# Performance work log

Hardware: AMD Instinct MI355X
Metric: run time of the kernel (lower is better)

The kernel has to match this reference:

```python
import jax, jax.numpy as jnp
import numpy as np

DIMS = [512, 256, 256, 256, 256, 256, 128, 128, 64, 40]
N_NODES = 100000
N_EDGES = 3200000


def setup_inputs() -> dict:
    key = jax.random.key(0)
    ks = jax.random.split(key, 4 + 2 * 9)
    inp = {
        "x": jax.random.normal(ks[0], (N_NODES, DIMS[0]), dtype=jnp.float32),
        "edge_src": jax.random.randint(ks[1], (N_EDGES,), 0, N_NODES, dtype=jnp.int32),
        "edge_dst": jax.random.randint(ks[2], (N_EDGES,), 0, N_NODES, dtype=jnp.int32),
        "edge_weight": jax.random.uniform(ks[3], (N_EDGES,), dtype=jnp.float32) / 32.0,
    }
    for i in range(9):
        fi, fo = DIMS[i], DIMS[i + 1]
        scale = 1.0 / np.sqrt(fi)
        inp[f"W{i+1}"] = jax.random.normal(ks[4 + 2 * i], (fi, fo), dtype=jnp.float32) * scale
        inp[f"b{i+1}"] = jax.random.normal(ks[5 + 2 * i], (fo,), dtype=jnp.float32) * scale
    return inp


def _gcn_layer(h, W, b, src, dst, w, n_nodes):
    # support = h @ W; out[i] = sum over edges (i <- j) of w * support[j] + b
    support = h @ W                          # [N, fo]
    msgs = w[:, None] * support[src]         # [E, fo] gather
    agg = jax.ops.segment_sum(msgs, dst, num_segments=n_nodes)  # [N, fo] scatter-add
    return agg + b


def reference(x, edge_src, edge_dst, edge_weight,
              W1, b1, W2, b2, W3, b3, W4, b4, W5, b5,
              W6, b6, W7, b7, W8, b8, W9, b9):
    n = x.shape[0]
    Ws = (W1, W2, W3, W4, W5, W6, W7, W8, W9)
    bs = (b1, b2, b3, b4, b5, b6, b7, b8, b9)
    h = x
    for i in range(8):  # layers 1..8 with ReLU
        h = jax.nn.relu(_gcn_layer(h, Ws[i], bs[i], edge_src, edge_dst, edge_weight, n))
    h = _gcn_layer(h, Ws[8], bs[8], edge_src, edge_dst, edge_weight, n)
    return jax.nn.log_softmax(h, axis=1)
```

## Files before the change

### kernel.cpp

```cpp
#include <hip/hip_runtime.h>
#include <cstdint>
#include <cstddef>

typedef __attribute__((ext_vector_type(8))) short bf16x8;
typedef __attribute__((ext_vector_type(4))) float f32x4;

static inline int cdiv(int a, int b) { return (a + b - 1) / b; }

__device__ inline unsigned short f2bf(float f) {
    union { float f; unsigned int u; } v; v.f = f;
    unsigned int u = v.u;
    return (unsigned short)((u + 0x7FFFu + ((u >> 16) & 1u)) >> 16);
}
__device__ inline float bf2f(unsigned short b) {
    union { unsigned int u; float f; } v; v.u = ((unsigned int)b) << 16;
    return v.f;
}

__device__ inline void fma16u(float* a, const int4& d, float ws) {
    const unsigned int dw[4] = {(unsigned)d.x, (unsigned)d.y, (unsigned)d.z, (unsigned)d.w};
#pragma unroll
    for (int w = 0; w < 4; ++w) {
        a[w * 4 + 0] += ws * (float)(dw[w] & 0xFFu);
        a[w * 4 + 1] += ws * (float)((dw[w] >> 8) & 0xFFu);
        a[w * 4 + 2] += ws * (float)((dw[w] >> 16) & 0xFFu);
        a[w * 4 + 3] += ws * (float)(dw[w] >> 24);
    }
}


struct TW {
    const float* W[9];
    int K[9];
    int N[9];
    int base[10];
    int nN;
};

__global__ __launch_bounds__(256) void prep_kernel(TW tw, unsigned short* __restrict__ Wt,
                                                   int* __restrict__ deg,
                                                   int* __restrict__ bucketCursor, int total) {
    int t = blockIdx.x * 256 + threadIdx.x;
    if (t < tw.nN) deg[t] = 0;
    if (t < 8) bucketCursor[t] = 0;
    if (t >= total) return;
    int l = 0;
#pragma unroll
    for (int i = 1; i <= 8; ++i)
        if (t >= tw.base[i]) l = i;
    int loc = t - tw.base[l];
    int K = tw.K[l], N = tw.N[l];
    int n = loc / K, k = loc - n * K;
    float v = (n < N) ? tw.W[l][(size_t)k * N + n] : 0.f;
    Wt[t] = f2bf(v);
}


#define PB_BLOCKS 2048

__global__ __launch_bounds__(256) void partition_v2(
        const int* __restrict__ src, const int* __restrict__ dst,
        const float* __restrict__ w,
        int* __restrict__ bucketCursor, int4* __restrict__ staging,
        int bucketCap, int nE, int nN) {
    __shared__ int cnt[8];
    __shared__ int cur[8];
    const int tid = threadIdx.x;
    const int lane = tid & 63;
    const int perBlock = (nE + (int)gridDim.x - 1) / (int)gridDim.x;
    const int begE = blockIdx.x * perBlock;
    const int endE = (begE + perBlock < nE) ? begE + perBlock : nE;
    if (begE >= endE) return;
    if (tid < 8) cnt[tid] = 0;
    __syncthreads();
    for (int i = begE + tid; i < endE; i += 256) {
        int d = dst[i];
        int b = (int)(((long long)d * 8) / nN);
#pragma unroll
        for (int bb = 0; bb < 8; ++bb) {
            unsigned long long mask = __ballot(b == bb);
            if (mask && lane == (__ffsll(mask) - 1))
                atomicAdd(&cnt[bb], (int)__popcll(mask));
        }
    }
    __syncthreads();
    if (tid < 8) cur[tid] = atomicAdd(&bucketCursor[tid], cnt[tid]);
    __syncthreads();
    for (int i = begE + tid; i < endE; i += 256) {
        int d = dst[i], s = src[i];
        float wv = w[i];
        int b = (int)(((long long)d * 8) / nN);
        int pos = 0;
#pragma unroll
        for (int bb = 0; bb < 8; ++bb) {
            unsigned long long mask = __ballot(b == bb);
            int leader = mask ? (__ffsll(mask) - 1) : 0;
            int base_bb = 0;
            if (mask && lane == leader) base_bb = atomicAdd(&cur[bb], (int)__popcll(mask));
            base_bb = __shfl(base_bb, leader);
            if (b == bb) pos = base_bb + (int)__popcll(mask & ((1ull << lane) - 1ull));
        }
        staging[(size_t)b * bucketCap + pos] = make_int4(d, s, __float_as_int(wv), 0);
    }
}


#define DC_BPB 32

__global__ __launch_bounds__(256) void deg_count(const int4* __restrict__ staging,
                                                 const int* __restrict__ bucketCnt,
                                                 int bucketCap, int* __restrict__ deg, int nN) {
    __shared__ int hist[12512];
    int bucket = blockIdx.x & 7;
    int chunk = blockIdx.x >> 3;
    int cnt = bucketCnt[bucket];
    int lo = (int)(((long long)bucket * nN + 7) / 8);
    int hi = (int)(((long long)(bucket + 1) * nN + 7) / 8);
    if (hi > nN) hi = nN;
    int span = hi - lo;
    for (int i = threadIdx.x; i < span; i += 256) hist[i] = 0;
    __syncthreads();
    const int4* st = staging + (size_t)bucket * bucketCap;
    for (int i = chunk * 256 + threadIdx.x; i < cnt; i += DC_BPB * 256)
        atomicAdd(&hist[st[i].x - lo], 1);
    __syncthreads();
    for (int i = threadIdx.x; i < span; i += 256) {
        int v = hist[i];
        if (v) atomicAdd(&deg[lo + i], v);
    }
}


__global__ __launch_bounds__(256) void scan_part(const int* __restrict__ deg,
                                                 int* __restrict__ partials, int n) {
    __shared__ int sdata[256];
    int tid = threadIdx.x;
    int base = blockIdx.x * 1024;
    int local = 0;
#pragma unroll
    for (int i = 0; i < 4; ++i) {
        int idx = base + tid * 4 + i;
        local += (idx < n) ? deg[idx] : 0;
    }
    sdata[tid] = local;
    __syncthreads();
    for (int off = 128; off; off >>= 1) {
        if (tid < off) sdata[tid] += sdata[tid + off];
        __syncthreads();
    }
    if (tid == 0) partials[blockIdx.x] = sdata[0];
}

__global__ __launch_bounds__(256) void scan_final2(const int* __restrict__ deg,
                                                   const int* __restrict__ partials,
                                                   int* __restrict__ rowptr,
                                                   int* __restrict__ cursor, int n, int nb) {
    __shared__ int ps[128];
    __shared__ int sdata[256];
    int tid = threadIdx.x;
    if (tid < 128) ps[tid] = (tid < nb) ? partials[tid] : 0;
    __syncthreads();
    for (int off = 1; off < 128; off <<= 1) {
        int t = (tid < 128 && tid >= off) ? ps[tid - off] : 0;
        __syncthreads();
        if (tid < 128) ps[tid] += t;
        __syncthreads();
    }
    int base = (blockIdx.x == 0) ? 0 : ps[blockIdx.x - 1];
    if (blockIdx.x == 0 && tid == 0) rowptr[n] = ps[nb - 1];
    int bb = blockIdx.x * 1024;
    int vals[4];
    int local = 0;
#pragma unroll
    for (int i = 0; i < 4; ++i) {
        int idx = bb + tid * 4 + i;
        vals[i] = (idx < n) ? deg[idx] : 0;
        local += vals[i];
    }
    sdata[tid] = local;
    __syncthreads();
    for (int off = 1; off < 256; off <<= 1) {
        int t = (tid >= off) ? sdata[tid - off] : 0;
        __syncthreads();
        sdata[tid] += t;
        __syncthreads();
    }
    int run = sdata[tid] - local + base;
#pragma unroll
    for (int i = 0; i < 4; ++i) {
        int idx = bb + tid * 4 + i;
        if (idx < n) { rowptr[idx] = run; cursor[idx] = run; }
        run += vals[i];
    }
}


__global__ __launch_bounds__(256) void scatter_b(const int4* __restrict__ staging,
                                                 const int* __restrict__ bucketCnt,
                                                 int bucketCap, int* __restrict__ cursor,
                                                 int2* __restrict__ ep, int blocksPerBucket) {
    int bucket = blockIdx.x & 7;
    int chunk = blockIdx.x >> 3;
    int cnt = bucketCnt[bucket];
    const int4* st = staging + (size_t)bucket * bucketCap;
    for (int i = chunk * 256 + threadIdx.x; i < cnt; i += blocksPerBucket * 256) {
        int4 r = st[i];
        int pos = atomicAdd(&cursor[r.x], 1);
        ep[pos] = make_int2(r.y, r.z);
    }
}


template <int BN, bool AF32, int OUTQ>
__global__ __launch_bounds__(256) void gemm_mfma(const void* __restrict__ Av,
                                                 const unsigned short* __restrict__ Bt,
                                                 void* __restrict__ Cv,
                                                 float* __restrict__ scArr,
                                                 int M, int K, int N) {
    constexpr int BM = 128, BK = 64;
    __shared__ unsigned short As[BM * BK];
    __shared__ unsigned short Bs[BN * BK];
    const int tid = threadIdx.x;
    const int lane = tid & 63, wid = tid >> 6;
    const int m0 = blockIdx.x * BM, n0 = blockIdx.y * BN;

    constexpr int WN = (BN == 128) ? 2 : 1;
    constexpr int WTM = (BN == 128) ? 64 : 32;
    constexpr int FM = WTM / 16, FN = 4;
    const int wm = (wid / WN) * WTM;
    const int wn = (wid % WN) * 64;
    const int g = lane >> 4, r16 = lane & 15;

    const unsigned short* A16 = (const unsigned short*)Av;
    const float* A32 = (const float*)Av;

    f32x4 acc[FM][FN] = {};

    for (int k0 = 0; k0 < K; k0 += BK) {
        if constexpr (AF32) {
#pragma unroll
            for (int it = 0; it < 4; ++it) {
                int c = it * 256 + tid;
                int r = c >> 3, kc = c & 7;
                int gm = m0 + r;
                bf16x8 val;
                if (gm < M) {
                    const float* p = A32 + (size_t)gm * K + k0 + kc * 8;
                    float4 v0 = *reinterpret_cast<const float4*>(p);
                    float4 v1 = *reinterpret_cast<const float4*>(p + 4);
                    val[0] = (short)f2bf(v0.x); val[1] = (short)f2bf(v0.y);
                    val[2] = (short)f2bf(v0.z); val[3] = (short)f2bf(v0.w);
                    val[4] = (short)f2bf(v1.x); val[5] = (short)f2bf(v1.y);
                    val[6] = (short)f2bf(v1.z); val[7] = (short)f2bf(v1.w);
                } else {
#pragma unroll
                    for (int j = 0; j < 8; ++j) val[j] = 0;
                }
                *reinterpret_cast<bf16x8*>(&As[r * BK + kc * 8]) = val;
            }
        } else {
#pragma unroll
            for (int c = 0; c < 4; ++c) {
                int base = wid * 32 + c * 8;
                int row = base + (lane >> 3), kc = lane & 7;
                const unsigned short* gp = A16 + (size_t)(m0 + row) * K + k0 + kc * 8;
                __builtin_amdgcn_global_load_lds(
                    (const __attribute__((address_space(1))) void*)gp,
                    (__attribute__((address_space(3))) void*)&As[base * BK], 16, 0, 0);
            }
        }
        {
            constexpr int BCALLS = (BN * BK) / (512 * 4);
#pragma unroll
            for (int c = 0; c < BCALLS; ++c) {
                int base = wid * (BN / 4) + c * 8;
                int row = base + (lane >> 3), kc = lane & 7;
                const unsigned short* gp = Bt + (size_t)(n0 + row) * K + k0 + kc * 8;
                __builtin_amdgcn_global_load_lds(
                    (const __attribute__((address_space(1))) void*)gp,
                    (__attribute__((address_space(3))) void*)&Bs[base * BK], 16, 0, 0);
            }
        }
        __syncthreads();
#pragma unroll
        for (int ks = 0; ks < 2; ++ks) {
            bf16x8 af[FM], bfr[FN];
#pragma unroll
            for (int i = 0; i < FM; ++i)
                af[i] = *reinterpret_cast<const bf16x8*>(&As[(wm + i * 16 + r16) * BK + ks * 32 + g * 8]);
#pragma unroll
            for (int j = 0; j < FN; ++j)
                bfr[j] = *reinterpret_cast<const bf16x8*>(&Bs[(wn + j * 16 + r16) * BK + ks * 32 + g * 8]);
#pragma unroll
            for (int i = 0; i < FM; ++i)
#pragma unroll
                for (int j = 0; j < FN; ++j)
                    acc[i][j] = __builtin_amdgcn_mfma_f32_16x16x32_bf16(af[i], bfr[j], acc[i][j], 0, 0, 0);
        }
        __syncthreads();
    }

    if constexpr (OUTQ == 1) {
        __shared__ float rmax2[2][BM];
        const int wc = wid % WN;
        unsigned char* C8 = (unsigned char*)Cv;
#pragma unroll
        for (int i = 0; i < FM; ++i) {
#pragma unroll
            for (int r = 0; r < 4; ++r) {
                float m = 0.f;
#pragma unroll
                for (int j = 0; j < FN; ++j) m = fmaxf(m, fabsf(acc[i][j][r]));
                m = fmaxf(m, __shfl_xor(m, 1));
                m = fmaxf(m, __shfl_xor(m, 2));
                m = fmaxf(m, __shfl_xor(m, 4));
                m = fmaxf(m, __shfl_xor(m, 8));
                if (r16 == 0) rmax2[wc][wm + i * 16 + g * 4 + r] = m;
            }
        }
        __syncthreads();
#pragma unroll
        for (int i = 0; i < FM; ++i) {
#pragma unroll
            for (int r = 0; r < 4; ++r) {
                int rl = wm + i * 16 + g * 4 + r;
                float rm = fmaxf(rmax2[0][rl], rmax2[1][rl]);
                float inv = (rm > 0.f) ? 127.f / rm : 0.f;
                int gm = m0 + rl;
                if (gm < M) {
                    if (wc == 0 && r16 == 0)
                        scArr[(size_t)gm * 2 + blockIdx.y] = rm * (1.f / 127.f);
#pragma unroll
                    for (int j = 0; j < FN; ++j) {
                        int gn = n0 + wn + j * 16 + r16;
                        float q = fminf(fmaxf(rintf(acc[i][j][r] * inv), -127.f), 127.f);
                        C8[(size_t)gm * N + gn] = (unsigned char)((int)q + 128);
                    }
                }
            }
        }
    } else if constexpr (OUTQ == 2) {
        unsigned char* C8 = (unsigned char*)Cv;
#pragma unroll
        for (int i = 0; i < FM; ++i) {
#pragma unroll
            for (int r = 0; r < 4; ++r) {
                float m = 0.f;
#pragma unroll
                for (int j = 0; j < FN; ++j) m = fmaxf(m, fabsf(acc[i][j][r]));
                m = fmaxf(m, __shfl_xor(m, 1));
                m = fmaxf(m, __shfl_xor(m, 2));
                m = fmaxf(m, __shfl_xor(m, 4));
                m = fmaxf(m, __shfl_xor(m, 8));
                float inv = (m > 0.f) ? 127.f / m : 0.f;
                int gm = m0 + wm + i * 16 + g * 4 + r;
                if (gm < M) {
                    if (r16 == 0) scArr[(size_t)gm * 2] = m * (1.f / 127.f);
#pragma unroll
                    for (int j = 0; j < FN; ++j) {
                        int gn = wn + j * 16 + r16;
                        float q = fminf(fmaxf(rintf(acc[i][j][r] * inv), -127.f), 127.f);
                        C8[(size_t)gm * 64 + gn] = (unsigned char)((int)q + 128);
                    }
                }
            }
        }
    } else {
        unsigned short* C = (unsigned short*)Cv;
#pragma unroll
        for (int i = 0; i < FM; ++i) {
            int gmBase = m0 + wm + i * 16 + g * 4;
#pragma unroll
            for (int j = 0; j < FN; ++j) {
                int gn = n0 + wn + j * 16 + r16;
                if (gn < N) {
#pragma unroll
                    for (int r = 0; r < 4; ++r) {
                        int gm = gmBase + r;
                        if (gm < M) C[(size_t)gm * N + gn] = f2bf(acc[i][j][r]);
                    }
                }
            }
        }
    }
}


template <int FO>
__global__ __launch_bounds__(256) void agg_q8(const char* __restrict__ supp8,
                                              const float* __restrict__ sc,
                                              const int2* __restrict__ ep,
                                              const int* __restrict__ rowptr,
                                              const float* __restrict__ bias,
                                              unsigned short* __restrict__ out, int n_nodes) {
    constexpr int LPR = FO / 16;
    constexpr int EPS = 64 / LPR;
    constexpr int G16 = 16 / EPS;
    constexpr int G8 = 8 / EPS;
    constexpr int TG = (FO == 256) ? 2 : 1;
    const int wave0 = (int)((blockIdx.x * blockDim.x + threadIdx.x) >> 6);
    const int nWaves = (int)((gridDim.x * blockDim.x) >> 6);
    const int lane = threadIdx.x & 63;
    const int lr = lane & (LPR - 1);
    const int half = lane / LPR;
    const int hi = (FO == 256) ? (lr >> 3) : 0;

    for (int node = wave0; node < n_nodes; node += nWaves) {
        int beg = __builtin_amdgcn_readfirstlane(rowptr[node]);
        int end = __builtin_amdgcn_readfirstlane(rowptr[node + 1]);
        float a[16] = {};
        float wsum = 0.f;
        int e = beg;
        for (; e + 16 <= end; e += 16) {
            int2 me[G16];
#pragma unroll
            for (int u = 0; u < G16; ++u) me[u] = ep[e + u * EPS + half];
            float ss[G16];
            int4 q[G16];
#pragma unroll
            for (int u = 0; u < G16; ++u) ss[u] = sc[(size_t)me[u].x * 2 + hi];
#pragma unroll
            for (int u = 0; u < G16; ++u)
                q[u] = *reinterpret_cast<const int4*>(supp8 + (size_t)me[u].x * FO + lr * 16);
#pragma unroll
            for (int u = 0; u < G16; ++u) {
                float ws = __int_as_float(me[u].y) * ss[u];
                fma16u(a, q[u], ws);
                wsum += ws;
            }
        }
        if constexpr (G8 >= 1) {
            for (; e + 8 <= end; e += 8) {
                int2 me[G8];
#pragma unroll
                for (int u = 0; u < G8; ++u) me[u] = ep[e + u * EPS + half];
                float ss[G8];
                int4 q[G8];
#pragma unroll
                for (int u = 0; u < G8; ++u) ss[u] = sc[(size_t)me[u].x * 2 + hi];
#pragma unroll
                for (int u = 0; u < G8; ++u)
                    q[u] = *reinterpret_cast<const int4*>(supp8 + (size_t)me[u].x * FO + lr * 16);
#pragma unroll
                for (int u = 0; u < G8; ++u) {
                    float ws = __int_as_float(me[u].y) * ss[u];
                    fma16u(a, q[u], ws);
                    wsum += ws;
                }
            }
        }
        {
            int rem = end - e;
            if (rem > 0) {
#pragma unroll
                for (int u = 0; u < TG; ++u) {
                    int idx = u * EPS + half;
                    bool ok = idx < rem;
                    int2 me = ep[e + (ok ? idx : 0)];
                    float ws = ok ? __int_as_float(me.y) * sc[(size_t)me.x * 2 + hi] : 0.f;
                    int4 q = *reinterpret_cast<const int4*>(supp8 + (size_t)me.x * FO + lr * 16);
                    fma16u(a, q, ws);
                    wsum += ws;
                }
            }
        }
#pragma unroll
        for (int j = 0; j < 16; ++j) a[j] -= 128.f * wsum;
#pragma unroll
        for (int off = LPR; off < 64; off <<= 1)
#pragma unroll
            for (int j = 0; j < 16; ++j) a[j] += __shfl_xor(a[j], off);
        if (lane < LPR) {
            float bb[16];
#pragma unroll
            for (int c = 0; c < 4; ++c) {
                float4 bv = *reinterpret_cast<const float4*>(bias + lr * 16 + c * 4);
                bb[c * 4 + 0] = bv.x; bb[c * 4 + 1] = bv.y;
                bb[c * 4 + 2] = bv.z; bb[c * 4 + 3] = bv.w;
            }
            bf16x8 o0, o1;
#pragma unroll
            for (int j = 0; j < 8; ++j) {
                o0[j] = (short)f2bf(fmaxf(a[j] + bb[j], 0.f));
                o1[j] = (short)f2bf(fmaxf(a[j + 8] + bb[j + 8], 0.f));
            }
            unsigned short* op = out + (size_t)node * FO + lr * 16;
            *reinterpret_cast<bf16x8*>(op) = o0;
            *reinterpret_cast<bf16x8*>(op + 8) = o1;
        }
    }
}


__global__ __launch_bounds__(256) void agg_lsm_kernel(const unsigned short* __restrict__ supp,
                                                      const int2* __restrict__ ep,
                                                      const int* __restrict__ rowptr,
                                                      const float* __restrict__ bias,
                                                      float* __restrict__ out, int n_nodes) {
    const int wave0 = (int)((blockIdx.x * blockDim.x + threadIdx.x) >> 6);
    const int nWaves = (int)((gridDim.x * blockDim.x) >> 6);
    const int lane = threadIdx.x & 63;
    const int lr = lane & 7;
    const int half = lane >> 3;

    for (int node = wave0; node < n_nodes; node += nWaves) {
        int beg = __builtin_amdgcn_readfirstlane(rowptr[node]);
        int end = __builtin_amdgcn_readfirstlane(rowptr[node + 1]);
        float a[8] = {};
        int e = beg;
        for (; e + 16 <= end; e += 16) {
            int2 me0 = ep[e + half];
            int2 me1 = ep[e + 8 + half];
            bf16x8 v0 = *reinterpret_cast<const bf16x8*>(supp + (size_t)me0.x * 64 + lr * 8);
            bf16x8 v1 = *reinterpret_cast<const bf16x8*>(supp + (size_t)me1.x * 64 + lr * 8);
            float w0 = __int_as_float(me0.y), w1 = __int_as_float(me1.y);
#pragma unroll
            for (int j = 0; j < 8; ++j)
                a[j] += w0 * bf2f((unsigned short)v0[j]) + w1 * bf2f((unsigned short)v1[j]);
        }
        {
            int rem = end - e;
            if (rem > 0) {
#pragma unroll
                for (int u = 0; u < 2; ++u) {
                    int idx = u * 8 + half;
                    bool ok = idx < rem;
                    int2 me = ep[e + (ok ? idx : 0)];
                    float wv = ok ? __int_as_float(me.y) : 0.f;
                    bf16x8 v = *reinterpret_cast<const bf16x8*>(supp + (size_t)me.x * 64 + lr * 8);
#pragma unroll
                    for (int j = 0; j < 8; ++j) a[j] += wv * bf2f((unsigned short)v[j]);
                }
            }
        }
#pragma unroll
        for (int off = 8; off < 64; off <<= 1)
#pragma unroll
            for (int j = 0; j < 8; ++j) a[j] += __shfl_xor(a[j], off);
        float vj[8];
#pragma unroll
        for (int j = 0; j < 8; ++j) {
            int col = lane * 8 + j;
            float bv = (lane < 8 && col < 40) ? bias[col] : 0.f;
            vj[j] = (col < 40) ? (a[j] + bv) : -1e30f;
        }
        float m = vj[0];
#pragma unroll
        for (int j = 1; j < 8; ++j) m = fmaxf(m, vj[j]);
#pragma unroll
        for (int off = 1; off < 8; off <<= 1) m = fmaxf(m, __shfl_xor(m, off));
        float s = 0.f;
#pragma unroll
        for (int j = 0; j < 8; ++j) s += expf(vj[j] - m);
#pragma unroll
        for (int off = 1; off < 8; off <<= 1) s += __shfl_xor(s, off);
        float ls = m + logf(s);
        if (lane < 5) {
            float4 o0, o1;
            o0.x = vj[0] - ls; o0.y = vj[1] - ls; o0.z = vj[2] - ls; o0.w = vj[3] - ls;
            o1.x = vj[4] - ls; o1.y = vj[5] - ls; o1.z = vj[6] - ls; o1.w = vj[7] - ls;
            float* op = out + (size_t)node * 40 + lane * 8;
            *reinterpret_cast<float4*>(op) = o0;
            *reinterpret_cast<float4*>(op + 4) = o1;
        }
    }
}


extern "C" void kernel_launch(void* const* d_in, const int* in_sizes, int n_in,
                              void* d_out, int out_size, void* d_ws, size_t ws_size,
                              hipStream_t stream) {
    const float* x    = (const float*)d_in[0];
    const int*   esrc = (const int*)d_in[1];
    const int*   edst = (const int*)d_in[2];
    const float* ew   = (const float*)d_in[3];

    const int nN = in_sizes[0] / 512;
    const int nE = in_sizes[1];

    const int dims[10] = {512, 256, 256, 256, 256, 256, 128, 128, 64, 40};
    const int BUCKET_CAP = ((nE / 8) + (nE / 64) + 4095) & ~4095;

    char* ws = (char*)d_ws;
    unsigned short* h    = (unsigned short*)ws;
    unsigned short* supp = (unsigned short*)(ws + (size_t)nN * 256 * 2);
    char* supp8 = (char*)supp;
    char* p = ws + (size_t)nN * 256 * 2 * 2;
    unsigned short* Wt = (unsigned short*)p; p += (1 << 21);
    float* scArr  = (float*)p; p += (size_t)nN * 2 * 4 + 256;
    int4* staging = (int4*)p; p += (size_t)8 * BUCKET_CAP * 16;
    int* deg      = (int*)p; p += ((size_t)nN + 64) * 4;
    int* rowptr   = (int*)p; p += ((size_t)nN + 64) * 4;
    int* cursor   = (int*)p; p += ((size_t)nN + 64) * 4;
    int* partials = (int*)p; p += 128 * 4;
    int* bucketCursor = (int*)p; p += 64 * 4;
    int2* ep      = (int2*)p; p += (size_t)nE * 8;

    TW tw;
    size_t woff[9];
    {
        int off = 0;
        for (int i = 0; i < 9; ++i) {
            tw.W[i] = (const float*)d_in[4 + 2 * i];
            tw.K[i] = dims[i];
            tw.N[i] = dims[i + 1];
            tw.base[i] = off;
            woff[i] = (size_t)off;
            int fop = cdiv(dims[i + 1], 64) * 64;
            off += fop * dims[i];
        }
        tw.base[9] = off;
        tw.nN = nN;
        int total = off;
        int nPrep = cdiv((total > nN + 8) ? total : nN + 8, 256);
        prep_kernel<<<nPrep, 256, 0, stream>>>(tw, Wt, deg, bucketCursor, total);
    }
    const float* b[9];
    for (int i = 0; i < 9; ++i) b[i] = (const float*)d_in[5 + 2 * i];

    partition_v2<<<PB_BLOCKS, 256, 0, stream>>>(esrc, edst, ew, bucketCursor,
                                                staging, BUCKET_CAP, nE, nN);
    deg_count<<<8 * DC_BPB, 256, 0, stream>>>(staging, bucketCursor, BUCKET_CAP, deg, nN);
    {
        int nb = cdiv(nN, 1024);
        scan_part<<<nb, 256, 0, stream>>>(deg, partials, nN);
        scan_final2<<<nb, 256, 0, stream>>>(deg, partials, rowptr, cursor, nN, nb);
    }
    scatter_b<<<8 * 256, 256, 0, stream>>>(staging, bucketCursor, BUCKET_CAP, cursor, ep, 256);

    const int aggBlocks = 2048;
    const int gBlocks = cdiv(nN, 128);

    const void* A = (const void*)x;
    for (int L = 0; L < 9; ++L) {
        int fi = dims[L], fo = dims[L + 1];
        if (L == 8) {
            dim3 g(gBlocks, 1);
            gemm_mfma<64, false, 0><<<g, 256, 0, stream>>>(A, Wt + woff[L], (void*)supp,
                                                           scArr, nN, fi, 64);
            agg_lsm_kernel<<<aggBlocks, 256, 0, stream>>>(supp, ep, rowptr, b[8], (float*)d_out, nN);
            break;
        }
        if (fo == 256) {
            dim3 g(gBlocks, 2);
            if (L == 0)
                gemm_mfma<128, true, 1><<<g, 256, 0, stream>>>(A, Wt + woff[L], (void*)supp8,
                                                               scArr, nN, fi, fo);
            else
                gemm_mfma<128, false, 1><<<g, 256, 0, stream>>>(A, Wt + woff[L], (void*)supp8,
                                                                scArr, nN, fi, fo);
            agg_q8<256><<<aggBlocks, 256, 0, stream>>>(supp8, scArr, ep, rowptr, b[L], h, nN);
        } else if (fo == 128) {
            dim3 g(gBlocks, 1);
            gemm_mfma<128, false, 1><<<g, 256, 0, stream>>>(A, Wt + woff[L], (void*)supp8,
                                                            scArr, nN, fi, fo);
            agg_q8<128><<<aggBlocks, 256, 0, stream>>>(supp8, scArr, ep, rowptr, b[L], h, nN);
        } else {
            dim3 g(gBlocks, 1);
            gemm_mfma<64, false, 2><<<g, 256, 0, stream>>>(A, Wt + woff[L], (void*)supp8,
                                                           scArr, nN, fi, 64);
            agg_q8<64><<<aggBlocks, 256, 0, stream>>>(supp8, scArr, ep, rowptr, b[L], h, nN);
        }
        A = (const void*)h;
    }
}
```

Baseline: 1.654 ms.

## Quantize last layer support to int8 and pre-convert input features to bf16

The final layer's support matrix now goes through the same 8-bit quantized path as earlier layers. A new aggregation kernel dequantizes with per-row scales and subtracts a 128·wsum offset before the log-softmax. When workspace allows, the fp32 input x is also converted once to bf16 so the first GEMM can use the bf16 A path instead of converting fp32 on the fly. The intent is to cut gather bandwidth in the last aggregation and the cost of the first-layer GEMM, at the price of an extra conversion pass over x and lower precision on the output logits.

```diff
diff --git a/kernel.cpp b/kernel.cpp
--- a/kernel.cpp
+++ b/kernel.cpp
@@ -21,6 +21,17 @@
     const unsigned int dw[4] = {(unsigned)d.x, (unsigned)d.y, (unsigned)d.z, (unsigned)d.w};
 #pragma unroll
     for (int w = 0; w < 4; ++w) {
+        a[w * 4 + 0] += ws * (float)(dw[w] & 0xFFu);
+        a[w * 4 + 1] += ws * (float)((dw[w] >> 8) & 0xFFu);
+        a[w * 4 + 2] += ws * (float)((dw[w] >> 16) & 0xFFu);
+        a[w * 4 + 3] += ws * (float)(dw[w] >> 24);
+    }
+}
+
+__device__ inline void fma8u(float* a, const int2& d, float ws) {
+    const unsigned int dw[2] = {(unsigned)d.x, (unsigned)d.y};
+#pragma unroll
+    for (int w = 0; w < 2; ++w) {
         a[w * 4 + 0] += ws * (float)(dw[w] & 0xFFu);
         a[w * 4 + 1] += ws * (float)((dw[w] >> 8) & 0xFFu);
         a[w * 4 + 2] += ws * (float)((dw[w] >> 16) & 0xFFu);
@@ -53,6 +64,23 @@
     int n = loc / K, k = loc - n * K;
     float v = (n < N) ? tw.W[l][(size_t)k * N + n] : 0.f;
     Wt[t] = f2bf(v);
+}
+
+
+__global__ __launch_bounds__(256) void cvt_x(const float* __restrict__ in,
+                                             unsigned short* __restrict__ out, int n8) {
+    int stride = gridDim.x * 256;
+    for (int i = blockIdx.x * 256 + threadIdx.x; i < n8; i += stride) {
+        const float* p = in + (size_t)i * 8;
+        float4 v0 = *reinterpret_cast<const float4*>(p);
+        float4 v1 = *reinterpret_cast<const float4*>(p + 4);
+        bf16x8 o;
+        o[0] = (short)f2bf(v0.x); o[1] = (short)f2bf(v0.y);
+        o[2] = (short)f2bf(v0.z); o[3] = (short)f2bf(v0.w);
+        o[4] = (short)f2bf(v1.x); o[5] = (short)f2bf(v1.y);
+        o[6] = (short)f2bf(v1.z); o[7] = (short)f2bf(v1.w);
+        *reinterpret_cast<bf16x8*>(out + (size_t)i * 8) = o;
+    }
 }
 
 
@@ -492,11 +520,12 @@
 }
 
 
-__global__ __launch_bounds__(256) void agg_lsm_kernel(const unsigned short* __restrict__ supp,
-                                                      const int2* __restrict__ ep,
-                                                      const int* __restrict__ rowptr,
-                                                      const float* __restrict__ bias,
-                                                      float* __restrict__ out, int n_nodes) {
+__global__ __launch_bounds__(256) void agg_lsm_q8(const char* __restrict__ supp8,
+                                                  const float* __restrict__ sc,
+                                                  const int2* __restrict__ ep,
+                                                  const int* __restrict__ rowptr,
+                                                  const float* __restrict__ bias,
+                                                  float* __restrict__ out, int n_nodes) {
     const int wave0 = (int)((blockIdx.x * blockDim.x + threadIdx.x) >> 6);
     const int nWaves = (int)((gridDim.x * blockDim.x) >> 6);
     const int lane = threadIdx.x & 63;
@@ -507,16 +536,20 @@
         int beg = __builtin_amdgcn_readfirstlane(rowptr[node]);
         int end = __builtin_amdgcn_readfirstlane(rowptr[node + 1]);
         float a[8] = {};
+        float wsum = 0.f;
         int e = beg;
         for (; e + 16 <= end; e += 16) {
             int2 me0 = ep[e + half];
             int2 me1 = ep[e + 8 + half];
-            bf16x8 v0 = *reinterpret_cast<const bf16x8*>(supp + (size_t)me0.x * 64 + lr * 8);
-            bf16x8 v1 = *reinterpret_cast<const bf16x8*>(supp + (size_t)me1.x * 64 + lr * 8);
-            float w0 = __int_as_float(me0.y), w1 = __int_as_float(me1.y);
-#pragma unroll
-            for (int j = 0; j < 8; ++j)
-                a[j] += w0 * bf2f((unsigned short)v0[j]) + w1 * bf2f((unsigned short)v1[j]);
+            float s0 = sc[(size_t)me0.x * 2];
+            float s1 = sc[(size_t)me1.x * 2];
+            int2 q0 = *reinterpret_cast<const int2*>(supp8 + (size_t)me0.x * 64 + lr * 8);
+            int2 q1 = *reinterpret_cast<const int2*>(supp8 + (size_t)me1.x * 64 + lr * 8);
+            float w0 = __int_as_float(me0.y) * s0;
+            float w1 = __int_as_float(me1.y) * s1;
+            fma8u(a, q0, w0);
+            fma8u(a, q1, w1);
+            wsum += w0 + w1;
         }
         {
             int rem = end - e;
@@ -526,17 +559,21 @@
                     int idx = u * 8 + half;
                     bool ok = idx < rem;
                     int2 me = ep[e + (ok ? idx : 0)];
-                    float wv = ok ? __int_as_float(me.y) : 0.f;
-                    bf16x8 v = *reinterpret_cast<const bf16x8*>(supp + (size_t)me.x * 64 + lr * 8);
-#pragma unroll
-                    for (int j = 0; j < 8; ++j) a[j] += wv * bf2f((unsigned short)v[j]);
+                    float ws = ok ? __int_as_float(me.y) * sc[(size_t)me.x * 2] : 0.f;
+                    int2 q = *reinterpret_cast<const int2*>(supp8 + (size_t)me.x * 64 + lr * 8);
+                    fma8u(a, q, ws);
+                    wsum += ws;
                 }
             }
         }
 #pragma unroll
-        for (int off = 8; off < 64; off <<= 1)
+        for (int off = 8; off < 64; off <<= 1) {
 #pragma unroll
             for (int j = 0; j < 8; ++j) a[j] += __shfl_xor(a[j], off);
+            wsum += __shfl_xor(wsum, off);
+        }
+#pragma unroll
+        for (int j = 0; j < 8; ++j) a[j] -= 128.f * wsum;
         float vj[8];
 #pragma unroll
         for (int j = 0; j < 8; ++j) {
@@ -581,13 +618,25 @@
     const int dims[10] = {512, 256, 256, 256, 256, 256, 128, 128, 64, 40};
     const int BUCKET_CAP = ((nE / 8) + (nE / 64) + 4095) & ~4095;
 
+    const size_t Sh    = (size_t)nN * 512;
+    const size_t Ssupp = (size_t)nN * 512;
+    const size_t Sxbf  = (size_t)nN * 1024;
+    const size_t Srest = (size_t)(1 << 21)
+                       + (size_t)nN * 8 + 256
+                       + (size_t)8 * BUCKET_CAP * 16
+                       + 3 * ((size_t)nN + 64) * 4
+                       + 128 * 4 + 64 * 4
+                       + (size_t)nE * 8;
+    const bool useXbf = ws_size >= Sh + Ssupp + Sxbf + Srest;
+
     char* ws = (char*)d_ws;
     unsigned short* h    = (unsigned short*)ws;
-    unsigned short* supp = (unsigned short*)(ws + (size_t)nN * 256 * 2);
+    unsigned short* supp = (unsigned short*)(ws + Sh);
     char* supp8 = (char*)supp;
-    char* p = ws + (size_t)nN * 256 * 2 * 2;
+    char* p = ws + Sh + Ssupp;
+    unsigned short* xbf = (unsigned short*)p; if (useXbf) p += Sxbf;
     unsigned short* Wt = (unsigned short*)p; p += (1 << 21);
-    float* scArr  = (float*)p; p += (size_t)nN * 2 * 4 + 256;
+    float* scArr  = (float*)p; p += (size_t)nN * 8 + 256;
     int4* staging = (int4*)p; p += (size_t)8 * BUCKET_CAP * 16;
     int* deg      = (int*)p; p += ((size_t)nN + 64) * 4;
     int* rowptr   = (int*)p; p += ((size_t)nN + 64) * 4;
@@ -618,6 +667,9 @@
     const float* b[9];
     for (int i = 0; i < 9; ++i) b[i] = (const float*)d_in[5 + 2 * i];
 
+    if (useXbf)
+        cvt_x<<<2048, 256, 0, stream>>>(x, xbf, nN * 64);
+
     partition_v2<<<PB_BLOCKS, 256, 0, stream>>>(esrc, edst, ew, bucketCursor,
                                                 staging, BUCKET_CAP, nE, nN);
     deg_count<<<8 * DC_BPB, 256, 0, stream>>>(staging, bucketCursor, BUCKET_CAP, deg, nN);
@@ -631,19 +683,20 @@
     const int aggBlocks = 2048;
     const int gBlocks = cdiv(nN, 128);
 
-    const void* A = (const void*)x;
+    const void* A = useXbf ? (const void*)xbf : (const void*)x;
     for (int L = 0; L < 9; ++L) {
         int fi = dims[L], fo = dims[L + 1];
         if (L == 8) {
             dim3 g(gBlocks, 1);
-            gemm_mfma<64, false, 0><<<g, 256, 0, stream>>>(A, Wt + woff[L], (void*)supp,
+            gemm_mfma<64, false, 2><<<g, 256, 0, stream>>>(A, Wt + woff[L], (void*)supp8,
                                                            scArr, nN, fi, 64);
-            agg_lsm_kernel<<<aggBlocks, 256, 0, stream>>>(supp, ep, rowptr, b[8], (float*)d_out, nN);
+            agg_lsm_q8<<<aggBlocks, 256, 0, stream>>>(supp8, scArr, ep, rowptr, b[8],
+                                                      (float*)d_out, nN);
             break;
         }
         if (fo == 256) {
             dim3 g(gBlocks, 2);
-            if (L == 0)
+            if (L == 0 && !useXbf)
                 gemm_mfma<128, true, 1><<<g, 256, 0, stream>>>(A, Wt + woff[L], (void*)supp8,
                                                                scArr, nN, fi, fo);
             else
```

Result: no change. 1.683 ms (+1.8%).
